# Kernel tuning notes

Hardware: AMD Instinct MI355X
Metric: run time of the kernel (lower is better)

## Reference

```python
import jax, jax.numpy as jnp
import numpy as np

BS, SEQ, IN, H = 16, 1024, 512, 512


def setup_inputs() -> dict:
    key = jax.random.key(0)
    ks = jax.random.split(key, 10)
    std = 1.0 / np.sqrt(H)
    u = lambda k, shape: jax.random.uniform(k, shape, jnp.float32, -std, std)
    return {
        "x": jax.random.normal(ks[0], (BS, SEQ, IN), jnp.float32),
        # input projection fc: input_size -> hidden_size
        "Wfc": u(ks[1], (IN, H)),
        "bfc": u(ks[2], (H,)),
        # cell 1 (main hidden stream h): tree of matmuls + gated elementwise
        "W1x": u(ks[3], (2 * H, H)),  # layer-0 cells see duplicated features (2H)
        "W1h": u(ks[4], (H, H)),
        "W1g": u(ks[5], (H, H)),
        # cell 2 (second hidden stream c)
        "W2x": u(ks[6], (2 * H, H)),
        "W2h": u(ks[7], (H, H)),
        "W2g": u(ks[8], (H, H)),
    }


def reference(x, Wfc, bfc, W1x, W1h, W1g, W2x, W2h, W2g):
    bs = x.shape[0]
    # layer-0 input prep: fc projection then feature duplication (cat([x,x],dim=2))
    xp = x @ Wfc + bfc                      # [bs, seq, H]
    xp = jnp.concatenate([xp, xp], axis=-1)  # [bs, seq, 2H]
    xs = jnp.swapaxes(xp, 0, 1)             # [seq, bs, 2H] for scan over time

    h0 = jnp.zeros((bs, H), x.dtype)
    c0 = jnp.zeros((bs, H), x.dtype)

    def step(carry, x_t):
        h, c = carry  # hidden streams x2, x3 fed to each evolved cell
        h_new = jnp.tanh(x_t @ W1x + h @ W1h + jax.nn.sigmoid(c @ W1g) * h)
        c_new = jax.nn.sigmoid(x_t @ W2x + c @ W2h) * jnp.tanh(h @ W2g)
        return (h_new, c_new), h_new  # hidden_seq collects stream 0

    (h_fin, c_fin), hseq = jax.lax.scan(step, (h0, c0), xs)
    out = jnp.swapaxes(hseq, 0, 1)  # batch_first: [bs, seq, H]
    # final hidden states: [num_layers*(1), bs, H] per main stream
    return out, h_fin[None], c_fin[None]
```

## Files before the change

kernel.cpp:

```cpp
#include <hip/hip_runtime.h>


typedef unsigned short u16;
typedef unsigned int   u32;
typedef __attribute__((ext_vector_type(8))) short s8v;
typedef __attribute__((ext_vector_type(4))) float f4v;

__device__ __forceinline__ u16 f2bf_rne(float f){
  u32 u = __float_as_uint(f);
  u32 r = u + 0x7fffu + ((u >> 16) & 1u);
  return (u16)(r >> 16);
}
__device__ __forceinline__ float bf2f(u16 h){ return __uint_as_float(((u32)h) << 16); }
__device__ __forceinline__ f4v MFMA(s8v a, s8v b, f4v c){
  return __builtin_amdgcn_mfma_f32_16x16x32_bf16(a, b, c, 0, 0, 0);
}
__device__ __forceinline__ float sigmoidf_(float x){ return 1.0f / (1.0f + __expf(-x)); }
__device__ __forceinline__ float tanh_fast(float x){
  float e = __expf(2.0f * x);
  return 1.0f - 2.0f / (e + 1.0f);
}

template<bool CC> __device__ __forceinline__ s8v ld16(const u16* p){
  s8v r;
  if (CC) asm volatile("global_load_dwordx4 %0, %1, off sc0 sc1" : "=v"(r) : "v"(p));
  else    asm volatile("global_load_dwordx4 %0, %1, off"         : "=v"(r) : "v"(p));
  return r;
}
template<bool CC> __device__ __forceinline__ void st2(u16* p, u32 v){
  if (CC) asm volatile("global_store_short %0, %1, off sc0 sc1" :: "v"(p), "v"(v) : "memory");
  else    asm volatile("global_store_short %0, %1, off"         :: "v"(p), "v"(v) : "memory");
}
__device__ __forceinline__ void store_dword_cc(u32* p, u32 v){
  asm volatile("global_store_dword %0, %1, off sc0 sc1" :: "v"(p), "v"(v) : "memory");
}
__device__ __forceinline__ void store_dword_plain_wait(u32* p, u32 v){
  asm volatile("global_store_dword %0, %1, off\n\ts_waitcnt vmcnt(0)"
               :: "v"(p), "v"(v) : "memory");
}
__device__ __forceinline__ u32 load_dword_plain_wait(const u32* p){
  u32 r;
  asm volatile("global_load_dword %0, %1, off\n\ts_waitcnt vmcnt(0)"
               : "=v"(r) : "v"(p));
  return r;
}

#define SEQT 1024
#define NWG  16
#define PROT 16

static const size_t OFF_U1  = 0;
static const size_t OFF_U2  = 33554432;
static const size_t OFF_WCT = OFF_U2 + 16777216;
static const size_t OFF_ST  = OFF_WCT;
static const size_t OFF_WT  = OFF_WCT + 1048576;
static const size_t OFF_BC  = OFF_WT + 2097152;
static const size_t OFF_FL  = OFF_BC + 4096;
static const size_t OFF_TOK = OFF_FL + 65536;
static const size_t OFF_PRS = OFF_TOK + 4096;
static const size_t OFF_CTL = OFF_PRS + 4096;
static const size_t OFF_CN  = OFF_CTL + 4096;
static const size_t OFF_HF2 = OFF_CN + 4096;
static const size_t OFF_CF2 = OFF_HF2 + 1048576;

__global__ void wcombk(const float* __restrict__ Wfc, const float* __restrict__ W1x,
                       const float* __restrict__ W2x, u16* __restrict__ Wct){
  __shared__ float A[16][17], B[16][17];
  const float* Wx = blockIdx.z ? W2x : W1x;
  int i0 = blockIdx.y * 16, n0 = blockIdx.x * 16;
  int tx = threadIdx.x, ty = threadIdx.y;
  float acc = 0.f;
  for (int kc = 0; kc < 512; kc += 16){
    A[ty][tx] = Wfc[(size_t)(i0 + ty) * 512 + kc + tx];
    B[ty][tx] = Wx[(size_t)(kc + ty) * 512 + n0 + tx]
              + Wx[(size_t)(kc + ty + 512) * 512 + n0 + tx];
    __syncthreads();
    #pragma unroll
    for (int kk = 0; kk < 16; ++kk) acc += A[ty][kk] * B[kk][tx];
    __syncthreads();
  }
  Wct[(size_t)(blockIdx.z * 512 + n0 + tx) * 512 + i0 + ty] = f2bf_rne(acc);
}

__global__ void bcombk(const float* __restrict__ bfc, const float* __restrict__ W1x,
                       const float* __restrict__ W2x, float* __restrict__ bc){
  int n = blockIdx.x * 256 + threadIdx.x;
  const float* Wx = (n < 512) ? W1x : W2x;
  int nl = n & 511;
  float acc = 0.f;
  for (int k = 0; k < 512; ++k)
    acc += bfc[k] * (Wx[(size_t)k * 512 + nl] + Wx[(size_t)(k + 512) * 512 + nl]);
  bc[n] = acc;
}

__global__ void wtk(const float* __restrict__ A, const float* __restrict__ B,
                    const float* __restrict__ C, const float* __restrict__ D,
                    u16* __restrict__ Wt){
  __shared__ float tile[32][33];
  const float* src = (blockIdx.z == 0) ? A : (blockIdx.z == 1) ? B
                    : (blockIdx.z == 2) ? C : D;
  int n0 = blockIdx.x * 32, k0 = blockIdx.y * 32;
  for (int i = threadIdx.y; i < 32; i += 8)
    tile[i][threadIdx.x] = src[(size_t)(k0 + i) * 512 + n0 + threadIdx.x];
  __syncthreads();
  for (int i = threadIdx.y; i < 32; i += 8)
    Wt[(size_t)blockIdx.z * 262144 + (size_t)(n0 + i) * 512 + k0 + threadIdx.x]
        = f2bf_rne(tile[threadIdx.x][i]);
}

__global__ __launch_bounds__(256) void gemmk(
    const float* __restrict__ x, const u16* __restrict__ Wct,
    const float* __restrict__ bc, float* __restrict__ U1, u16* __restrict__ U2){
  int l = threadIdx.x & 63, w = threadIdx.x >> 6;
  int lr = l & 15, lk = l >> 4;
  int m0 = blockIdx.y * 128 + (w & 1) * 64;
  int n0 = blockIdx.x * 64 + (w >> 1) * 32;
  f4v acc[4][2] = {};
  for (int ks = 0; ks < 16; ++ks){
    int k0 = ks * 32 + lk * 8;
    s8v bh0 = *(const s8v*)(Wct + (size_t)(n0 + lr) * 512 + k0);
    s8v bh1 = *(const s8v*)(Wct + (size_t)(n0 + 16 + lr) * 512 + k0);
    #pragma unroll
    for (int mi = 0; mi < 4; ++mi){
      const float* xp = x + (size_t)(m0 + mi * 16 + lr) * 512 + k0;
      f4v v0 = *(const f4v*)xp;
      f4v v1 = *(const f4v*)(xp + 4);
      s8v ah, al;
      #pragma unroll
      for (int j = 0; j < 4; ++j){
        { u32 u = __float_as_uint(v0[j]); ah[j] = (short)(u >> 16);
          float lof = v0[j] - __uint_as_float(u & 0xffff0000u);
          al[j] = (short)(__float_as_uint(lof) >> 16); }
        { u32 u = __float_as_uint(v1[j]); ah[j + 4] = (short)(u >> 16);
          float lof = v1[j] - __uint_as_float(u & 0xffff0000u);
          al[j + 4] = (short)(__float_as_uint(lof) >> 16); }
      }
      acc[mi][0] = MFMA(ah, bh0, acc[mi][0]);
      acc[mi][0] = MFMA(al, bh0, acc[mi][0]);
      acc[mi][1] = MFMA(ah, bh1, acc[mi][1]);
      acc[mi][1] = MFMA(al, bh1, acc[mi][1]);
    }
  }
  #pragma unroll
  for (int mi = 0; mi < 4; ++mi)
    #pragma unroll
    for (int ni = 0; ni < 2; ++ni){
      int n = n0 + ni * 16 + lr;
      float badd = bc[n];
      #pragma unroll
      for (int j = 0; j < 4; ++j){
        int r = m0 + mi * 16 + lk * 4 + j;
        int b = r >> 10, t = r & 1023;
        size_t oi = (size_t)(t * 16 + b) * 512;
        float v = acc[mi][ni][j] + badd;
        if (n < 512) U1[oi + n] = v;
        else         U2[oi + n - 512] = f2bf_rne(v);
      }
    }
}

__device__ __forceinline__ void scan_fast(
    int wg, int tid,
    const float* __restrict__ U1, const u16* __restrict__ U2,
    const u16* __restrict__ Wt, u16* __restrict__ st,
    u32* __restrict__ hfl, u32* __restrict__ cfl,
    float* __restrict__ out, float* xg, float* xt){
  const int w = tid >> 6, l = tid & 63;
  const int lr = l & 15, lk = l >> 4;
  const int ncol0 = wg * 32 + lr;

  s8v bf0[16], bf1[16];
  {
    const u16* Wm = Wt + (size_t)w * (512 * 512);
    #pragma unroll
    for (int ks = 0; ks < 16; ++ks){
      bf0[ks] = *(const s8v*)(Wm + (size_t)ncol0 * 512 + ks * 32 + lk * 8);
      bf1[ks] = *(const s8v*)(Wm + (size_t)(ncol0 + 16) * 512 + ks * 32 + lk * 8);
    }
  }
  const bool useH = (w == 0) || (w == 3);
  u32* myfl = useH ? hfl : cfl;
  float hp0[4] = {0, 0, 0, 0}, hp1[4] = {0, 0, 0, 0};

  float un0[4], un1[4], uc0[4], uc1[4];
  u32   ur0[4], ur1[4];
  if (w == 0){
    #pragma unroll
    for (int j = 0; j < 4; ++j){
      size_t ro = (size_t)(lk * 4 + j) * 512;
      un0[j] = U1[ro + ncol0];
      un1[j] = U1[ro + ncol0 + 16];
    }
  } else if (w == 2){
    #pragma unroll
    for (int j = 0; j < 4; ++j){
      size_t ro = (size_t)(lk * 4 + j) * 512;
      ur0[j] = U2[ro + ncol0];
      ur1[j] = U2[ro + ncol0 + 16];
    }
  }

  for (int t = 0; t < SEQT; ++t){
    if (t > 0){
      u32* fl = myfl + (size_t)(t - 1) * (NWG * 16);
      u32 seen = (l < NWG) ? 0u : 1u;
      int g2 = 0;
      for (;;){
        if (!seen){
          u32 v = __hip_atomic_fetch_add(fl + l * 16, 0x10000u,
                                         __ATOMIC_RELAXED, __HIP_MEMORY_SCOPE_WORKGROUP);
          if ((v & 0xffffu) != 0u) seen = 1u;
        }
        if (__all(seen != 0u)) break;
        if (++g2 > 2000000) break;
      }
      __builtin_amdgcn_sched_barrier(0);
    }
    u16* rb = st + (size_t)(t & (PROT - 1)) * 32768 + (useH ? 0 : 16384);
    s8v ah[16], al[16];
    {
      u16* bhp = rb + lr * 512 + lk * 8;
      u16* blp = rb + 8192 + lr * 512 + lk * 8;
      #pragma unroll
      for (int ks = 0; ks < 16; ++ks){
        ah[ks] = ld16<false>(bhp + ks * 32);
        al[ks] = ld16<false>(blp + ks * 32);
      }
    }
    asm volatile("s_waitcnt vmcnt(0)" ::: "memory");
    __builtin_amdgcn_sched_barrier(0);

    if (w == 0){
      #pragma unroll
      for (int j = 0; j < 4; ++j){ uc0[j] = un0[j]; uc1[j] = un1[j]; }
    } else if (w == 2){
      #pragma unroll
      for (int j = 0; j < 4; ++j){
        uc0[j] = __uint_as_float(ur0[j] << 16);
        uc1[j] = __uint_as_float(ur1[j] << 16);
      }
    }

    f4v a0 = {0, 0, 0, 0}, a1 = {0, 0, 0, 0};
    f4v b0 = {0, 0, 0, 0}, b1 = {0, 0, 0, 0};
    #pragma unroll
    for (int ks = 0; ks < 16; ++ks){
      a0 = MFMA(ah[ks], bf0[ks], a0);
      a1 = MFMA(ah[ks], bf1[ks], a1);
      b0 = MFMA(al[ks], bf0[ks], b0);
      b1 = MFMA(al[ks], bf1[ks], b1);
    }
    #pragma unroll
    for (int j = 0; j < 4; ++j){ a0[j] += b0[j]; a1[j] += b1[j]; }

    const int par = t & 1;
    if (w == 1){
      #pragma unroll
      for (int j = 0; j < 4; ++j){
        xg[((par * 2 + 0) * 16 + lk * 4 + j) * 16 + lr] = sigmoidf_(a0[j]);
        xg[((par * 2 + 1) * 16 + lk * 4 + j) * 16 + lr] = sigmoidf_(a1[j]);
      }
    } else if (w == 3){
      #pragma unroll
      for (int j = 0; j < 4; ++j){
        xt[((par * 2 + 0) * 16 + lk * 4 + j) * 16 + lr] = tanh_fast(a0[j]);
        xt[((par * 2 + 1) * 16 + lk * 4 + j) * 16 + lr] = tanh_fast(a1[j]);
      }
    }
    __syncthreads();
    u16* wb = st + (size_t)((t + 1) & (PROT - 1)) * 32768;
    const int tn = (t + 1 < SEQT) ? t + 1 : t;
    if (w == 0){
      float hn0v[4], hn1v[4];
      #pragma unroll
      for (int j = 0; j < 4; ++j){
        int b = lk * 4 + j;
        float hn0 = tanh_fast(uc0[j] + a0[j] + xg[((par * 2 + 0) * 16 + b) * 16 + lr] * hp0[j]);
        float hn1 = tanh_fast(uc1[j] + a1[j] + xg[((par * 2 + 1) * 16 + b) * 16 + lr] * hp1[j]);
        hp0[j] = hn0; hp1[j] = hn1;
        hn0v[j] = hn0; hn1v[j] = hn1;
        u32 u0 = __float_as_uint(hn0), u1 = __float_as_uint(hn1);
        int bi = b * 512;
        st2<false>(wb + bi + ncol0,      u0 >> 16);
        st2<false>(wb + bi + ncol0 + 16, u1 >> 16);
        float lo0 = hn0 - __uint_as_float(u0 & 0xffff0000u);
        float lo1 = hn1 - __uint_as_float(u1 & 0xffff0000u);
        st2<false>(wb + 8192 + bi + ncol0,      __float_as_uint(lo0) >> 16);
        st2<false>(wb + 8192 + bi + ncol0 + 16, __float_as_uint(lo1) >> 16);
      }
      #pragma unroll
      for (int j = 0; j < 4; ++j){
        size_t ro = (size_t)(tn * 16 + lk * 4 + j) * 512;
        un0[j] = U1[ro + ncol0];
        un1[j] = U1[ro + ncol0 + 16];
      }
      asm volatile("s_waitcnt vmcnt(8)" ::: "memory");
      if (l == 0)
        __hip_atomic_fetch_add(hfl + (size_t)t * (NWG * 16) + wg * 16, 1u,
                               __ATOMIC_RELAXED, __HIP_MEMORY_SCOPE_WORKGROUP);
      #pragma unroll
      for (int j = 0; j < 4; ++j){
        int b = lk * 4 + j;
        size_t ob = (size_t)b * (SEQT * 512) + (size_t)t * 512;
        out[ob + ncol0]      = hn0v[j];
        out[ob + ncol0 + 16] = hn1v[j];
        if (t == SEQT - 1){
          out[8388608 + (size_t)b * 512 + ncol0]      = hn0v[j];
          out[8388608 + (size_t)b * 512 + ncol0 + 16] = hn1v[j];
        }
      }
    } else if (w == 2){
      float cn0v[4], cn1v[4];
      #pragma unroll
      for (int j = 0; j < 4; ++j){
        int b = lk * 4 + j;
        float cn0 = sigmoidf_(uc0[j] + a0[j]) * xt[((par * 2 + 0) * 16 + b) * 16 + lr];
        float cn1 = sigmoidf_(uc1[j] + a1[j]) * xt[((par * 2 + 1) * 16 + b) * 16 + lr];
        cn0v[j] = cn0; cn1v[j] = cn1;
        u32 u0 = __float_as_uint(cn0), u1 = __float_as_uint(cn1);
        int bi = b * 512;
        st2<false>(wb + 16384 + bi + ncol0,      u0 >> 16);
        st2<false>(wb + 16384 + bi + ncol0 + 16, u1 >> 16);
        float lo0 = cn0 - __uint_as_float(u0 & 0xffff0000u);
        float lo1 = cn1 - __uint_as_float(u1 & 0xffff0000u);
        st2<false>(wb + 24576 + bi + ncol0,      __float_as_uint(lo0) >> 16);
        st2<false>(wb + 24576 + bi + ncol0 + 16, __float_as_uint(lo1) >> 16);
      }
      #pragma unroll
      for (int j = 0; j < 4; ++j){
        size_t ro = (size_t)(tn * 16 + lk * 4 + j) * 512;
        ur0[j] = U2[ro + ncol0];
        ur1[j] = U2[ro + ncol0 + 16];
      }
      asm volatile("s_waitcnt vmcnt(8)" ::: "memory");
      if (l == 0)
        __hip_atomic_fetch_add(cfl + (size_t)t * (NWG * 16) + wg * 16, 1u,
                               __ATOMIC_RELAXED, __HIP_MEMORY_SCOPE_WORKGROUP);
      if (t == SEQT - 1){
        #pragma unroll
        for (int j = 0; j < 4; ++j){
          int b = lk * 4 + j;
          out[8396800 + (size_t)b * 512 + ncol0]      = cn0v[j];
          out[8396800 + (size_t)b * 512 + ncol0 + 16] = cn1v[j];
        }
      }
    }
  }
}

__device__ __forceinline__ void scan_cc(
    int wg, int tid,
    const float* __restrict__ U1, const u16* __restrict__ U2,
    const u16* __restrict__ Wt, u16* __restrict__ st,
    u32* __restrict__ flags, float* __restrict__ out, float* xg, float* xt){
  const int w = tid >> 6, l = tid & 63;
  const int lr = l & 15, lk = l >> 4;
  const int ncol0 = wg * 32 + lr;
  s8v bf0[16], bf1[16];
  {
    const u16* Wm = Wt + (size_t)w * (512 * 512);
    #pragma unroll
    for (int ks = 0; ks < 16; ++ks){
      bf0[ks] = *(const s8v*)(Wm + (size_t)ncol0 * 512 + ks * 32 + lk * 8);
      bf1[ks] = *(const s8v*)(Wm + (size_t)(ncol0 + 16) * 512 + ks * 32 + lk * 8);
    }
  }
  const bool useH = (w == 0) || (w == 3);
  float hp0[4] = {0, 0, 0, 0}, hp1[4] = {0, 0, 0, 0};
  long guard = 0;
  for (int t = 0; t < SEQT; ++t){
    float uu0[4], uu1[4];
    if (w == 0){
      #pragma unroll
      for (int j = 0; j < 4; ++j){
        size_t ro = (size_t)(t * 16 + lk * 4 + j) * 512;
        uu0[j] = U1[ro + ncol0];
        uu1[j] = U1[ro + ncol0 + 16];
      }
    } else if (w == 2){
      #pragma unroll
      for (int j = 0; j < 4; ++j){
        size_t ro = (size_t)(t * 16 + lk * 4 + j) * 512;
        uu0[j] = bf2f(U2[ro + ncol0]);
        uu1[j] = bf2f(U2[ro + ncol0 + 16]);
      }
    }
    if (t > 0){
      const u32* fl = flags + (size_t)(t - 1) * NWG;
      for (;;){
        u32 v = 1u;
        if (l < NWG) v = __hip_atomic_load(fl + l, __ATOMIC_RELAXED, __HIP_MEMORY_SCOPE_AGENT);
        if (__all(v != 0u)) break;
        if (++guard > 1000000L) break;
      }
      __builtin_amdgcn_sched_barrier(0);
    }
    u16* rb = st + (size_t)(t & (PROT - 1)) * 32768 + (useH ? 0 : 16384);
    s8v ah[16], al[16];
    {
      u16* bhp = rb + lr * 512 + lk * 8;
      u16* blp = rb + 8192 + lr * 512 + lk * 8;
      #pragma unroll
      for (int ks = 0; ks < 16; ++ks){
        ah[ks] = ld16<true>(bhp + ks * 32);
        al[ks] = ld16<true>(blp + ks * 32);
      }
    }
    asm volatile("s_waitcnt vmcnt(0)" ::: "memory");
    __builtin_amdgcn_sched_barrier(0);
    f4v a0 = {0, 0, 0, 0}, a1 = {0, 0, 0, 0};
    f4v b0 = {0, 0, 0, 0}, b1 = {0, 0, 0, 0};
    #pragma unroll
    for (int ks = 0; ks < 16; ++ks){
      a0 = MFMA(ah[ks], bf0[ks], a0);
      a1 = MFMA(ah[ks], bf1[ks], a1);
      b0 = MFMA(al[ks], bf0[ks], b0);
      b1 = MFMA(al[ks], bf1[ks], b1);
    }
    #pragma unroll
    for (int j = 0; j < 4; ++j){ a0[j] += b0[j]; a1[j] += b1[j]; }
    if (w == 1){
      #pragma unroll
      for (int j = 0; j < 4; ++j){
        xg[(0 * 16 + lk * 4 + j) * 16 + lr] = sigmoidf_(a0[j]);
        xg[(1 * 16 + lk * 4 + j) * 16 + lr] = sigmoidf_(a1[j]);
      }
    } else if (w == 3){
      #pragma unroll
      for (int j = 0; j < 4; ++j){
        xt[(0 * 16 + lk * 4 + j) * 16 + lr] = tanh_fast(a0[j]);
        xt[(1 * 16 + lk * 4 + j) * 16 + lr] = tanh_fast(a1[j]);
      }
    }
    __syncthreads();
    u16* wb = st + (size_t)((t + 1) & (PROT - 1)) * 32768;
    float hn0v[4], hn1v[4], cn0v[4], cn1v[4];
    if (w == 0){
      #pragma unroll
      for (int j = 0; j < 4; ++j){
        int b = lk * 4 + j;
        float hn0 = tanh_fast(uu0[j] + a0[j] + xg[(0 * 16 + b) * 16 + lr] * hp0[j]);
        float hn1 = tanh_fast(uu1[j] + a1[j] + xg[(1 * 16 + b) * 16 + lr] * hp1[j]);
        hp0[j] = hn0; hp1[j] = hn1;
        hn0v[j] = hn0; hn1v[j] = hn1;
        u32 u0 = __float_as_uint(hn0), u1 = __float_as_uint(hn1);
        int bi = b * 512;
        st2<true>(wb + bi + ncol0,      u0 >> 16);
        st2<true>(wb + bi + ncol0 + 16, u1 >> 16);
        float lo0 = hn0 - __uint_as_float(u0 & 0xffff0000u);
        float lo1 = hn1 - __uint_as_float(u1 & 0xffff0000u);
        st2<true>(wb + 8192 + bi + ncol0,      __float_as_uint(lo0) >> 16);
        st2<true>(wb + 8192 + bi + ncol0 + 16, __float_as_uint(lo1) >> 16);
      }
      asm volatile("s_waitcnt vmcnt(0)" ::: "memory");
    } else if (w == 2){
      #pragma unroll
      for (int j = 0; j < 4; ++j){
        int b = lk * 4 + j;
        float cn0 = sigmoidf_(uu0[j] + a0[j]) * xt[(0 * 16 + b) * 16 + lr];
        float cn1 = sigmoidf_(uu1[j] + a1[j]) * xt[(1 * 16 + b) * 16 + lr];
        cn0v[j] = cn0; cn1v[j] = cn1;
        u32 u0 = __float_as_uint(cn0), u1 = __float_as_uint(cn1);
        int bi = b * 512;
        st2<true>(wb + 16384 + bi + ncol0,      u0 >> 16);
        st2<true>(wb + 16384 + bi + ncol0 + 16, u1 >> 16);
        float lo0 = cn0 - __uint_as_float(u0 & 0xffff0000u);
        float lo1 = cn1 - __uint_as_float(u1 & 0xffff0000u);
        st2<true>(wb + 24576 + bi + ncol0,      __float_as_uint(lo0) >> 16);
        st2<true>(wb + 24576 + bi + ncol0 + 16, __float_as_uint(lo1) >> 16);
      }
      asm volatile("s_waitcnt vmcnt(0)" ::: "memory");
    }
    __syncthreads();
    if (tid == 0) store_dword_cc(flags + (size_t)t * NWG + wg, 1u);
    if (w == 0){
      #pragma unroll
      for (int j = 0; j < 4; ++j){
        int b = lk * 4 + j;
        size_t ob = (size_t)b * (SEQT * 512) + (size_t)t * 512;
        out[ob + ncol0]      = hn0v[j];
        out[ob + ncol0 + 16] = hn1v[j];
        if (t == SEQT - 1){
          out[8388608 + (size_t)b * 512 + ncol0]      = hn0v[j];
          out[8388608 + (size_t)b * 512 + ncol0 + 16] = hn1v[j];
        }
      }
    } else if (w == 2 && t == SEQT - 1){
      #pragma unroll
      for (int j = 0; j < 4; ++j){
        int b = lk * 4 + j;
        out[8396800 + (size_t)b * 512 + ncol0]      = cn0v[j];
        out[8396800 + (size_t)b * 512 + ncol0 + 16] = cn1v[j];
      }
    }
  }
}

__global__ __launch_bounds__(256, 1) void recurk(
    const float* __restrict__ U1, const u16* __restrict__ U2,
    const u16* __restrict__ Wt, u16* __restrict__ st,
    u32* __restrict__ flags, u32* __restrict__ hfl, u32* __restrict__ cfl,
    u32* __restrict__ tok, u32* __restrict__ prs,
    u32* __restrict__ ctl, float* __restrict__ out){
  const int tid = threadIdx.x;
  __shared__ int slot_sh, mode_sh;
  __shared__ float xg[4 * 16 * 16], xt[4 * 16 * 16];
  u32* cntp  = ctl;
  u32* modep = ctl + 16;

  if (tid == 0){
    int s = -1;
    u32 xcc;
    asm volatile("s_getreg_b32 %0, hwreg(HW_REG_XCC_ID)" : "=s"(xcc));
    if ((xcc & 0xfu) == 0u)
      s = (int)__hip_atomic_fetch_add(cntp, 1u, __ATOMIC_RELAXED,
                                      __HIP_MEMORY_SCOPE_AGENT);
    slot_sh = s;
  }
  __syncthreads();
  const int slot = slot_sh;

  if (tid == 0){
    if (slot >= 0 && slot < NWG){
      store_dword_plain_wait(tok + slot * 16, 0x5A5A0000u + (u32)slot);
      __hip_atomic_store(prs + slot * 16, 1u, __ATOMIC_RELAXED,
                         __HIP_MEMORY_SCOPE_AGENT);
    }
    if (blockIdx.x == 0){
      long g = 0;
      for (;;){
        u32 c = __hip_atomic_load(cntp, __ATOMIC_RELAXED, __HIP_MEMORY_SCOPE_AGENT);
        if (c >= NWG) break;
        if (++g > 2000000L){ atomicCAS(modep, 0u, 2u); break; }
      }
    }
    if (slot == 0){
      bool ok = true;
      long g = 0;
      for (int s2 = 1; s2 < NWG && ok; ++s2){
        for (;;){
          u32 p = __hip_atomic_load(prs + s2 * 16, __ATOMIC_RELAXED,
                                    __HIP_MEMORY_SCOPE_AGENT);
          if (p) break;
          if (++g > 5000000L){ ok = false; break; }
        }
      }
      if (ok){
        for (int s2 = 1; s2 < NWG; ++s2){
          u32 v = load_dword_plain_wait(tok + s2 * 16);
          if (v != 0x5A5A0000u + (u32)s2){ ok = false; break; }
        }
      }
      atomicCAS(modep, 0u, ok ? 1u : 3u);
    }
    long g = 0;
    u32 m;
    for (;;){
      m = __hip_atomic_load(modep, __ATOMIC_RELAXED, __HIP_MEMORY_SCOPE_AGENT);
      if (m) break;
      if (++g > 50000000L){ m = 3u; break; }
    }
    mode_sh = (int)m;
  }
  __syncthreads();
  const int mode = mode_sh;

  int wg; bool part;
  if (mode == 2){ wg = blockIdx.x; part = (wg < NWG); }
  else          { wg = slot;       part = (slot >= 0 && slot < NWG); }
  if (!part) return;

  if (mode == 1) scan_fast(wg, tid, U1, U2, Wt, st, hfl, cfl, out, xg, xt);
  else           scan_cc (wg, tid, U1, U2, Wt, st, flags, out, xg, xt);
}

extern "C" void kernel_launch(void* const* d_in, const int* in_sizes, int n_in,
                              void* d_out, int out_size, void* d_ws, size_t ws_size,
                              hipStream_t stream){
  const float* x   = (const float*)d_in[0];
  const float* Wfc = (const float*)d_in[1];
  const float* bfc = (const float*)d_in[2];
  const float* W1x = (const float*)d_in[3];
  const float* W1h = (const float*)d_in[4];
  const float* W1g = (const float*)d_in[5];
  const float* W2x = (const float*)d_in[6];
  const float* W2h = (const float*)d_in[7];
  const float* W2g = (const float*)d_in[8];

  char* ws = (char*)d_ws;
  float* U1   = (float*)(ws + OFF_U1);
  u16*   U2   = (u16*)  (ws + OFF_U2);
  u16*   Wct  = (u16*)  (ws + OFF_WCT);
  u16*   st   = (u16*)  (ws + OFF_ST);
  u16*   Wt   = (u16*)  (ws + OFF_WT);
  float* bc   = (float*)(ws + OFF_BC);
  u32*   flags= (u32*)  (ws + OFF_FL);
  u32*   tok  = (u32*)  (ws + OFF_TOK);
  u32*   prs  = (u32*)  (ws + OFF_PRS);
  u32*   ctl  = (u32*)  (ws + OFF_CTL);
  u32*   hfl  = (u32*)  (ws + OFF_HF2);
  u32*   cfl  = (u32*)  (ws + OFF_CF2);
  float* out  = (float*)d_out;

  hipMemsetAsync(ws + OFF_FL, 0, 65536 + 4096 + 4096 + 4096 + 4096, stream);
  hipMemsetAsync(ws + OFF_HF2, 0, 2097152, stream);

  wcombk<<<dim3(32, 32, 2), dim3(16, 16), 0, stream>>>(Wfc, W1x, W2x, Wct);
  bcombk<<<dim3(4), dim3(256), 0, stream>>>(bfc, W1x, W2x, bc);
  wtk   <<<dim3(16, 16, 4), dim3(32, 8), 0, stream>>>(W1h, W1g, W2h, W2g, Wt);
  gemmk <<<dim3(16, 128), dim3(256), 0, stream>>>(x, Wct, bc, U1, U2);
  hipMemsetAsync(ws + OFF_ST, 0, 1048576, stream);
  recurk<<<dim3(256), dim3(256), 0, stream>>>(U1, U2, Wt, st, flags, hfl, cfl, tok, prs, ctl, out);
}
```

Baseline: 7.268 ms.

## Replace per-WG flag polling with shared counters and intra-block LDS tokens

The per-step grid synchronisation changes. Previously every wave polled 16 per-workgroup flags; now one lane of a single producer wave (w0 or w2) polls one counter per step with s_sleep backoff. Other waves are released through LDS tokens instead of __syncthreads, and the block-wide barrier between gate computation and state update becomes point-to-point token waits. The aim is less atomic traffic and less barrier stall on the serial critical path. The cost is atomic contention on a single counter, and the added sleep may add wake-up latency.

Measured after the change: 6.245 ms, median of 2. -14.1%, faster.

```diff
diff --git a/kernel.cpp b/kernel.cpp
--- a/kernel.cpp
+++ b/kernel.cpp
@@ -60,8 +60,8 @@
 static const size_t OFF_PRS = OFF_TOK + 4096;
 static const size_t OFF_CTL = OFF_PRS + 4096;
 static const size_t OFF_CN  = OFF_CTL + 4096;
-static const size_t OFF_HF2 = OFF_CN + 4096;
-static const size_t OFF_CF2 = OFF_HF2 + 1048576;
+static const size_t OFF_HCN = OFF_CN + 4096;
+static const size_t OFF_CCN = OFF_HCN + 131072;
 
 __global__ void wcombk(const float* __restrict__ Wfc, const float* __restrict__ W1x,
                        const float* __restrict__ W2x, u16* __restrict__ Wct){
@@ -159,12 +159,35 @@
     }
 }
 
+__device__ __forceinline__ void poll_cnt(u32* p, u32 need, int l){
+  int g = 0;
+  for (;;){
+    u32 v = 0;
+    if (l == 0)
+      v = __hip_atomic_fetch_add(p, 0x10000u, __ATOMIC_RELAXED,
+                                 __HIP_MEMORY_SCOPE_WORKGROUP);
+    v = __builtin_amdgcn_readfirstlane(v);
+    if ((v & 0xffffu) >= need) break;
+    if (++g > 4000000) break;
+    __builtin_amdgcn_s_sleep(1);
+  }
+}
+__device__ __forceinline__ void tok_store(u32* tok, u32 v){
+  __hip_atomic_store(tok, v, __ATOMIC_RELEASE, __HIP_MEMORY_SCOPE_WORKGROUP);
+}
+__device__ __forceinline__ void spin_tok(u32* tok, u32 need){
+  int g = 0;
+  while (__hip_atomic_load(tok, __ATOMIC_ACQUIRE, __HIP_MEMORY_SCOPE_WORKGROUP) < need){
+    if (++g > 16000000) break;
+  }
+}
+
 __device__ __forceinline__ void scan_fast(
     int wg, int tid,
     const float* __restrict__ U1, const u16* __restrict__ U2,
     const u16* __restrict__ Wt, u16* __restrict__ st,
-    u32* __restrict__ hfl, u32* __restrict__ cfl,
-    float* __restrict__ out, float* xg, float* xt){
+    u32* __restrict__ hcnt, u32* __restrict__ ccnt,
+    float* __restrict__ out, float* xg, float* xt, u32* ltok){
   const int w = tid >> 6, l = tid & 63;
   const int lr = l & 15, lk = l >> 4;
   const int ncol0 = wg * 32 + lr;
@@ -179,7 +202,6 @@
     }
   }
   const bool useH = (w == 0) || (w == 3);
-  u32* myfl = useH ? hfl : cfl;
   float hp0[4] = {0, 0, 0, 0}, hp1[4] = {0, 0, 0, 0};
 
   float un0[4], un1[4], uc0[4], uc1[4];
@@ -201,21 +223,19 @@
   }
 
   for (int t = 0; t < SEQT; ++t){
-    if (t > 0){
-      u32* fl = myfl + (size_t)(t - 1) * (NWG * 16);
-      u32 seen = (l < NWG) ? 0u : 1u;
-      int g2 = 0;
-      for (;;){
-        if (!seen){
-          u32 v = __hip_atomic_fetch_add(fl + l * 16, 0x10000u,
-                                         __ATOMIC_RELAXED, __HIP_MEMORY_SCOPE_WORKGROUP);
-          if ((v & 0xffffu) != 0u) seen = 1u;
-        }
-        if (__all(seen != 0u)) break;
-        if (++g2 > 2000000) break;
-      }
-      __builtin_amdgcn_sched_barrier(0);
-    }
+    if (w == 0){
+      if (t > 0) poll_cnt(hcnt + (size_t)(t - 1) * 32, NWG, l);
+      tok_store(ltok + 0, (u32)(t + 1));
+    } else if (w == 2){
+      if (t > 0) poll_cnt(ccnt + (size_t)(t - 1) * 32, NWG, l);
+      tok_store(ltok + 1, (u32)(t + 1));
+    } else if (w == 3){
+      spin_tok(ltok + 0, (u32)(t + 1));
+    } else {
+      spin_tok(ltok + 1, (u32)(t + 1));
+    }
+    __builtin_amdgcn_sched_barrier(0);
+
     u16* rb = st + (size_t)(t & (PROT - 1)) * 32768 + (useH ? 0 : 16384);
     s8v ah[16], al[16];
     {
@@ -254,23 +274,26 @@
     for (int j = 0; j < 4; ++j){ a0[j] += b0[j]; a1[j] += b1[j]; }
 
     const int par = t & 1;
+    u16* wb = st + (size_t)((t + 1) & (PROT - 1)) * 32768;
+    const int tn = (t + 1 < SEQT) ? t + 1 : t;
+
     if (w == 1){
       #pragma unroll
       for (int j = 0; j < 4; ++j){
         xg[((par * 2 + 0) * 16 + lk * 4 + j) * 16 + lr] = sigmoidf_(a0[j]);
         xg[((par * 2 + 1) * 16 + lk * 4 + j) * 16 + lr] = sigmoidf_(a1[j]);
       }
+      tok_store(ltok + 2, (u32)(t + 1));
     } else if (w == 3){
       #pragma unroll
       for (int j = 0; j < 4; ++j){
         xt[((par * 2 + 0) * 16 + lk * 4 + j) * 16 + lr] = tanh_fast(a0[j]);
         xt[((par * 2 + 1) * 16 + lk * 4 + j) * 16 + lr] = tanh_fast(a1[j]);
       }
-    }
-    __syncthreads();
-    u16* wb = st + (size_t)((t + 1) & (PROT - 1)) * 32768;
-    const int tn = (t + 1 < SEQT) ? t + 1 : t;
-    if (w == 0){
+      tok_store(ltok + 3, (u32)(t + 1));
+    } else if (w == 0){
+      spin_tok(ltok + 2, (u32)(t + 1));
+      __builtin_amdgcn_sched_barrier(0);
       float hn0v[4], hn1v[4];
       #pragma unroll
       for (int j = 0; j < 4; ++j){
@@ -296,7 +319,7 @@
       }
       asm volatile("s_waitcnt vmcnt(8)" ::: "memory");
       if (l == 0)
-        __hip_atomic_fetch_add(hfl + (size_t)t * (NWG * 16) + wg * 16, 1u,
+        __hip_atomic_fetch_add(hcnt + (size_t)t * 32, 1u,
                                __ATOMIC_RELAXED, __HIP_MEMORY_SCOPE_WORKGROUP);
       #pragma unroll
       for (int j = 0; j < 4; ++j){
@@ -309,7 +332,9 @@
           out[8388608 + (size_t)b * 512 + ncol0 + 16] = hn1v[j];
         }
       }
-    } else if (w == 2){
+    } else {
+      spin_tok(ltok + 3, (u32)(t + 1));
+      __builtin_amdgcn_sched_barrier(0);
       float cn0v[4], cn1v[4];
       #pragma unroll
       for (int j = 0; j < 4; ++j){
@@ -334,7 +359,7 @@
       }
       asm volatile("s_waitcnt vmcnt(8)" ::: "memory");
       if (l == 0)
-        __hip_atomic_fetch_add(cfl + (size_t)t * (NWG * 16) + wg * 16, 1u,
+        __hip_atomic_fetch_add(ccnt + (size_t)t * 32, 1u,
                                __ATOMIC_RELAXED, __HIP_MEMORY_SCOPE_WORKGROUP);
       if (t == SEQT - 1){
         #pragma unroll
@@ -499,12 +524,13 @@
 __global__ __launch_bounds__(256, 1) void recurk(
     const float* __restrict__ U1, const u16* __restrict__ U2,
     const u16* __restrict__ Wt, u16* __restrict__ st,
-    u32* __restrict__ flags, u32* __restrict__ hfl, u32* __restrict__ cfl,
+    u32* __restrict__ flags, u32* __restrict__ hcnt, u32* __restrict__ ccnt,
     u32* __restrict__ tok, u32* __restrict__ prs,
     u32* __restrict__ ctl, float* __restrict__ out){
   const int tid = threadIdx.x;
   __shared__ int slot_sh, mode_sh;
   __shared__ float xg[4 * 16 * 16], xt[4 * 16 * 16];
+  __shared__ u32 ltok[4];
   u32* cntp  = ctl;
   u32* modep = ctl + 16;
 
@@ -562,6 +588,7 @@
     }
     mode_sh = (int)m;
   }
+  if (tid < 4) ltok[tid] = 0;
   __syncthreads();
   const int mode = mode_sh;
 
@@ -570,7 +597,7 @@
   else          { wg = slot;       part = (slot >= 0 && slot < NWG); }
   if (!part) return;
 
-  if (mode == 1) scan_fast(wg, tid, U1, U2, Wt, st, hfl, cfl, out, xg, xt);
+  if (mode == 1) scan_fast(wg, tid, U1, U2, Wt, st, hcnt, ccnt, out, xg, xt, ltok);
   else           scan_cc (wg, tid, U1, U2, Wt, st, flags, out, xg, xt);
 }
 
@@ -598,17 +625,17 @@
   u32*   tok  = (u32*)  (ws + OFF_TOK);
   u32*   prs  = (u32*)  (ws + OFF_PRS);
   u32*   ctl  = (u32*)  (ws + OFF_CTL);
-  u32*   hfl  = (u32*)  (ws + OFF_HF2);
-  u32*   cfl  = (u32*)  (ws + OFF_CF2);
+  u32*   hcnt = (u32*)  (ws + OFF_HCN);
+  u32*   ccnt = (u32*)  (ws + OFF_CCN);
   float* out  = (float*)d_out;
 
   hipMemsetAsync(ws + OFF_FL, 0, 65536 + 4096 + 4096 + 4096 + 4096, stream);
-  hipMemsetAsync(ws + OFF_HF2, 0, 2097152, stream);
+  hipMemsetAsync(ws + OFF_HCN, 0, 262144, stream);
 
   wcombk<<<dim3(32, 32, 2), dim3(16, 16), 0, stream>>>(Wfc, W1x, W2x, Wct);
   bcombk<<<dim3(4), dim3(256), 0, stream>>>(bfc, W1x, W2x, bc);
   wtk   <<<dim3(16, 16, 4), dim3(32, 8), 0, stream>>>(W1h, W1g, W2h, W2g, Wt);
   gemmk <<<dim3(16, 128), dim3(256), 0, stream>>>(x, Wct, bc, U1, U2);
   hipMemsetAsync(ws + OFF_ST, 0, 1048576, stream);
-  recurk<<<dim3(256), dim3(256), 0, stream>>>(U1, U2, Wt, st, flags, hfl, cfl, tok, prs, ctl, out);
-}
+  recurk<<<dim3(256), dim3(256), 0, stream>>>(U1, U2, Wt, st, flags, hcnt, ccnt, tok, prs, ctl, out);
+}
```
